# Kernel optimization log

Hardware: AMD Instinct MI355X
Metric: run time of the kernel (lower is better)

Reference implementation:

```python
import jax, jax.numpy as jnp
import numpy as np

DIM = 1024
INTER = 1408
N_EXPERTS = 16
TOPK = 2
N_SHARED = 2
SHARED_INTER = N_SHARED * INTER
ROUTE_SCALE = 1.0


def setup_inputs() -> dict:
    key = jax.random.key(0)
    ks = jax.random.split(key, 16)
    s = 0.02
    return {
        "x": jax.random.normal(ks[0], (2, 2048, DIM), dtype=jnp.float32),
        "gate_w": jax.random.normal(ks[1], (DIM, N_EXPERTS), dtype=jnp.float32) * s,
        "gate_b": jnp.zeros((N_EXPERTS,), dtype=jnp.float32),
        "w1": jax.random.normal(ks[2], (N_EXPERTS, DIM, INTER), dtype=jnp.float32) * s,
        "b1": jnp.zeros((N_EXPERTS, INTER), dtype=jnp.float32),
        "w3": jax.random.normal(ks[3], (N_EXPERTS, DIM, INTER), dtype=jnp.float32) * s,
        "b3": jnp.zeros((N_EXPERTS, INTER), dtype=jnp.float32),
        "w2": jax.random.normal(ks[4], (N_EXPERTS, INTER, DIM), dtype=jnp.float32) * s,
        "b2": jnp.zeros((N_EXPERTS, DIM), dtype=jnp.float32),
        "sw1": jax.random.normal(ks[5], (DIM, SHARED_INTER), dtype=jnp.float32) * s,
        "sb1": jax.random.normal(ks[6], (SHARED_INTER,), dtype=jnp.float32) * s,
        "sw3": jax.random.normal(ks[7], (DIM, SHARED_INTER), dtype=jnp.float32) * s,
        "sb3": jax.random.normal(ks[8], (SHARED_INTER,), dtype=jnp.float32) * s,
        "sw2": jax.random.normal(ks[9], (SHARED_INTER, DIM), dtype=jnp.float32) * s,
        "sb2": jax.random.normal(ks[10], (DIM,), dtype=jnp.float32) * s,
    }


def reference(x, gate_w, gate_b, w1, b1, w3, b3, w2, b2, sw1, sb1, sw3, sb3, sw2, sb2):
    shape = x.shape
    xf = x.reshape(-1, DIM)  # [T, D]

    # Gate: softmax scores in fp32, top-k routing
    logits = xf @ gate_w + gate_b  # [T, E]
    scores = jax.nn.softmax(logits.astype(jnp.float32), axis=-1)
    top_vals, top_idx = jax.lax.top_k(scores, TOPK)  # [T, K]
    weights = (top_vals * ROUTE_SCALE).astype(x.dtype)

    # Combine weights per expert: [T, E]; zero for unselected experts
    cw = (jax.nn.one_hot(top_idx, N_EXPERTS, dtype=x.dtype) * weights[..., None]).sum(axis=1)

    # Routed experts (dense-per-expert SwiGLU, masked by combine weights)
    h = jnp.einsum('td,edh->teh', xf, w1) + b1  # [T, E, I]
    g = jnp.einsum('td,edh->teh', xf, w3) + b3
    a = jax.nn.silu(h) * g
    y = jnp.einsum('teh,ehd,te->td', a, w2, cw) + cw @ b2  # [T, D]

    # Shared expert SwiGLU
    z = (jax.nn.silu(xf @ sw1 + sb1) * (xf @ sw3 + sb3)) @ sw2 + sb2

    return (y + z).reshape(shape)
```

## Files before the change

### kernel.cpp

```cpp
#include <hip/hip_runtime.h>
#include <cstdint>
#include <cstddef>

#define T_TOKENS 4096
#define DIM      1024
#define INTER    1408
#define NEXP     16
#define SINTER   2816

typedef uint32_t u32;
typedef uint16_t u16;

using s8v = __attribute__((ext_vector_type(8))) short;
using f4v = __attribute__((ext_vector_type(4))) float;

__device__ __forceinline__ u16 f2bf(float f) {
  u32 u = __float_as_uint(f);
  return (u16)((u + 0x7fffu + ((u >> 16) & 1u)) >> 16);
}
__device__ __forceinline__ u32 pack2(float a, float b) {
  return (u32)f2bf(a) | ((u32)f2bf(b) << 16);
}

__device__ __forceinline__ void load_lds16(const u16* g, u16* l) {
  __builtin_amdgcn_global_load_lds((const __attribute__((address_space(1))) void*)g,
                                   (__attribute__((address_space(3))) void*)l,
                                   16, 0, 0);
}

__global__ __launch_bounds__(256)
void cvt_x(const float* __restrict__ in, u16* __restrict__ out) {
  const int i = (blockIdx.x * 256 + threadIdx.x) * 8;
  float4 a = *(const float4*)(in + i);
  float4 b = *(const float4*)(in + i + 4);
  uint4 o;
  o.x = pack2(a.x, a.y); o.y = pack2(a.z, a.w);
  o.z = pack2(b.x, b.y); o.w = pack2(b.z, b.w);
  *(uint4*)(out + i) = o;
}

__global__ __launch_bounds__(256)
void transpose_cvt(const float* __restrict__ in, u16* __restrict__ out,
                   int K, int N) {
  const size_t eoff = (size_t)blockIdx.z * K * N;
  const int n0 = blockIdx.x * 64, k0 = blockIdx.y * 64;
  __shared__ u16 t[64][72];

  const int tid = threadIdx.x;
  {
    const int r = tid >> 4, c4 = (tid & 15) * 4;
    const float* src = in + eoff + (size_t)k0 * N + n0;
#pragma unroll
    for (int i = 0; i < 4; i++) {
      int row = r + i * 16;
      float4 v = *(const float4*)(src + (size_t)row * N + c4);
      t[c4 + 0][row] = f2bf(v.x);
      t[c4 + 1][row] = f2bf(v.y);
      t[c4 + 2][row] = f2bf(v.z);
      t[c4 + 3][row] = f2bf(v.w);
    }
  }
  __syncthreads();
  {
    const int r = tid >> 3, cc = (tid & 7) * 8;
    u16* dst = out + eoff + (size_t)n0 * K + k0;
#pragma unroll
    for (int i = 0; i < 2; i++) {
      int row = r + i * 32;
      uint4 v = *(const uint4*)&t[row][cc];
      *(uint4*)(dst + (size_t)row * K + cc) = v;
    }
  }
}

__global__ __launch_bounds__(256)
void gate_logits(const float* __restrict__ x, const float* __restrict__ gw,
                 const float* __restrict__ gb,
                 int* __restrict__ g_e, float* __restrict__ g_w)
{
  const int tok  = blockIdx.x * 4 + (threadIdx.x >> 6);
  const int lane = threadIdx.x & 63;
  const int e = lane & 15, s = lane >> 4;
  const float* xr = x + (size_t)tok * DIM;

  float acc = 0.f;
#pragma unroll 8
  for (int i = 0; i < DIM / 4; i++) {
    const int k = i * 4 + s;
    acc = fmaf(xr[k], gw[i * 64 + lane], acc);
  }
  acc += __shfl_xor(acc, 16, 64);
  acc += __shfl_xor(acc, 32, 64);
  const float logit = acc + gb[e];

  float mx = logit;
#pragma unroll
  for (int o = 1; o < 16; o <<= 1) mx = fmaxf(mx, __shfl_xor(mx, o, 64));
  float p = __expf(logit - mx);
  float sum = p;
#pragma unroll
  for (int o = 1; o < 16; o <<= 1) sum += __shfl_xor(sum, o, 64);
  p /= sum;

  float m0 = p; int i0 = e;
#pragma unroll
  for (int o = 1; o < 16; o <<= 1) {
    float om = __shfl_xor(m0, o, 64); int oi = __shfl_xor(i0, o, 64);
    if (om > m0 || (om == m0 && oi < i0)) { m0 = om; i0 = oi; }
  }
  float p1 = (e == i0) ? -1.f : p;
  float m1 = p1; int i1 = e;
#pragma unroll
  for (int o = 1; o < 16; o <<= 1) {
    float om = __shfl_xor(m1, o, 64); int oi = __shfl_xor(i1, o, 64);
    if (om > m1 || (om == m1 && oi < i1)) { m1 = om; i1 = oi; }
  }
  if (lane == 0) {
    g_e[tok * 2 + 0] = i0;  g_e[tok * 2 + 1] = i1;
    g_w[tok * 2 + 0] = m0;  g_w[tok * 2 + 1] = m1;
  }
}

__global__ __launch_bounds__(256)
void route_build(const int* __restrict__ g_e, const float* __restrict__ g_w,
                 int* __restrict__ offsets,
                 int* __restrict__ tok_slot, float* __restrict__ w_slot)
{
  __shared__ int hist[256][NEXP + 1];
  __shared__ int base[NEXP + 1];
  const int tid = threadIdx.x;
  const int TPT = T_TOKENS / 256;
  const int t0 = tid * TPT;

#pragma unroll
  for (int e = 0; e < NEXP; e++) hist[tid][e] = 0;
  for (int t = t0; t < t0 + TPT; t++) {
    hist[tid][g_e[t * 2 + 0]]++;
    hist[tid][g_e[t * 2 + 1]]++;
  }
  __syncthreads();
  if (tid < NEXP) {
    int run = 0;
    for (int i = 0; i < 256; i++) { int v = hist[i][tid]; hist[i][tid] = run; run += v; }
    base[tid] = run;
  }
  __syncthreads();
  if (tid == 0) {
    int run = 0;
#pragma unroll
    for (int e = 0; e < NEXP; e++) { int c = base[e]; base[e] = run; offsets[e] = run; run += c; }
    base[NEXP] = run; offsets[NEXP] = run;
  }
  __syncthreads();
  for (int t = t0; t < t0 + TPT; t++) {
#pragma unroll
    for (int k = 0; k < 2; k++) {
      const int e = g_e[t * 2 + k];
      const int slot = base[e] + hist[tid][e]++;
      tok_slot[slot] = t;
      w_slot[slot] = g_w[t * 2 + k];
    }
  }
}

template<bool GATHER>
__global__ __launch_bounds__(256, 2)
void ffn_up2(const u16* __restrict__ xbf,
             const u16* __restrict__ w1t, const float* __restrict__ b1p,
             const u16* __restrict__ w3t, const float* __restrict__ b3p,
             int N,
             const int* __restrict__ offsets, const int* __restrict__ tok_slot,
             u16* __restrict__ act)
{
  int e = 0, rowbase = 0, count = T_TOKENS;
  if constexpr (GATHER) {
    e = blockIdx.z; rowbase = offsets[e]; count = offsets[e + 1] - rowbase;
  }
  const int m0 = blockIdx.y * 128;
  if (m0 >= count) return;
  const int n0 = blockIdx.x * 128;

  const u16* W1 = w1t + (size_t)e * N * DIM;
  const u16* W3 = w3t + (size_t)e * N * DIM;
  const float* B1 = b1p + (size_t)e * N;
  const float* B3 = b3p + (size_t)e * N;

  __shared__ u16 sA[128 * 32];
  __shared__ u16 sB1[128 * 32];
  __shared__ u16 sB3[128 * 32];

  const int tid = threadIdx.x;
  const int lane = tid & 63;
  const int w = tid >> 6;

  const int kc8 = (lane & 3) * 8;
  const u16* aptr[2]; const u16* b1ptr[2]; const u16* b3ptr[2];
  u16 *ldsA[2], *ldsB1[2], *ldsB3[2];
#pragma unroll
  for (int i = 0; i < 2; i++) {
    const int row = i * 64 + w * 16 + (lane >> 2);
    const int ldoff = i * 2048 + w * 512 + lane * 8;
    ldsA[i] = sA + ldoff; ldsB1[i] = sB1 + ldoff; ldsB3[i] = sB3 + ldoff;
    int arow = m0 + row; if (arow > count - 1) arow = count - 1;
    const int tok = GATHER ? tok_slot[rowbase + arow] : arow;
    aptr[i]  = xbf + (size_t)tok * DIM + kc8;
    const int brow = n0 + row;
    b1ptr[i] = W1 + (size_t)brow * DIM + kc8;
    b3ptr[i] = W3 + (size_t)brow * DIM + kc8;
  }

  const int ln = lane & 15, q = lane >> 4;
  const int wm = (w & 1) * 64, wn = (w >> 1) * 64;
  const u16* pa  = sA  + (wm + ln) * 32 + q * 8;
  const u16* pb1 = sB1 + (wn + ln) * 32 + q * 8;
  const u16* pb3 = sB3 + (wn + ln) * 32 + q * 8;

  f4v acc1[4][4] = {};
  f4v acc3[4][4] = {};

  for (int k0 = 0; k0 < DIM; k0 += 32) {
    __syncthreads();
#pragma unroll
    for (int i = 0; i < 2; i++) {
      load_lds16(aptr[i]  + k0, ldsA[i]);
      load_lds16(b1ptr[i] + k0, ldsB1[i]);
      load_lds16(b3ptr[i] + k0, ldsB3[i]);
    }
    __syncthreads();

    s8v af[4];
#pragma unroll
    for (int i = 0; i < 4; i++) af[i] = *(const s8v*)(pa + i * 512);
#pragma unroll
    for (int j = 0; j < 4; j++) {
      s8v bf1 = *(const s8v*)(pb1 + j * 512);
#pragma unroll
      for (int i = 0; i < 4; i++)
        acc1[i][j] = __builtin_amdgcn_mfma_f32_16x16x32_bf16(af[i], bf1, acc1[i][j], 0, 0, 0);
      s8v bf3 = *(const s8v*)(pb3 + j * 512);
#pragma unroll
      for (int i = 0; i < 4; i++)
        acc3[i][j] = __builtin_amdgcn_mfma_f32_16x16x32_bf16(af[i], bf3, acc3[i][j], 0, 0, 0);
    }
  }

  float bb1[4], bb3[4];
#pragma unroll
  for (int j = 0; j < 4; j++) {
    const int col = n0 + wn + j * 16 + ln;
    bb1[j] = B1[col]; bb3[j] = B3[col];
  }
#pragma unroll
  for (int i = 0; i < 4; i++) {
#pragma unroll
    for (int r = 0; r < 4; r++) {
      const int row = m0 + wm + i * 16 + q * 4 + r;
      if (row >= count) continue;
      u16* ap = act + (size_t)(rowbase + row) * N + n0 + wn;
#pragma unroll
      for (int j = 0; j < 4; j++) {
        float h = acc1[i][j][r] + bb1[j];
        float g = acc3[i][j][r] + bb3[j];
        float sv = 1.f / (1.f + __expf(-h));
        ap[j * 16 + ln] = f2bf(h * sv * g);
      }
    }
  }
}

template<bool SCATTER>
__global__ __launch_bounds__(256, 2)
void ffn_down2(const u16* __restrict__ act, int KA,
               const u16* __restrict__ w2t, const float* __restrict__ b2p,
               const int* __restrict__ offsets, const int* __restrict__ tok_slot,
               const float* __restrict__ w_slot, float* __restrict__ out)
{
  int e = 0, rowbase = 0, count = T_TOKENS;
  if constexpr (SCATTER) {
    e = blockIdx.z; rowbase = offsets[e]; count = offsets[e + 1] - rowbase;
  }
  const int m0 = blockIdx.y * 128;
  if (m0 >= count) return;
  const int n0 = blockIdx.x * 128;

  const u16* W2 = w2t + (size_t)e * DIM * KA;
  const float* B2 = b2p + (size_t)e * DIM;

  __shared__ u16 sA[128 * 32];
  __shared__ u16 sB[128 * 32];

  const int tid = threadIdx.x;
  const int lane = tid & 63;
  const int w = tid >> 6;

  const int kc8 = (lane & 3) * 8;
  const u16* aptr[2]; const u16* bptr[2];
  u16 *ldsA[2], *ldsB[2];
#pragma unroll
  for (int i = 0; i < 2; i++) {
    const int row = i * 64 + w * 16 + (lane >> 2);
    const int ldoff = i * 2048 + w * 512 + lane * 8;
    ldsA[i] = sA + ldoff; ldsB[i] = sB + ldoff;
    int arow = m0 + row; if (arow > count - 1) arow = count - 1;
    aptr[i] = act + (size_t)(rowbase + arow) * KA + kc8;
    bptr[i] = W2 + (size_t)(n0 + row) * KA + kc8;
  }

  const int ln = lane & 15, q = lane >> 4;
  const int wm = (w & 1) * 64, wn = (w >> 1) * 64;
  const u16* pa = sA + (wm + ln) * 32 + q * 8;
  const u16* pb = sB + (wn + ln) * 32 + q * 8;

  f4v acc[4][4] = {};

  for (int k0 = 0; k0 < KA; k0 += 32) {
    __syncthreads();
#pragma unroll
    for (int i = 0; i < 2; i++) {
      load_lds16(aptr[i] + k0, ldsA[i]);
      load_lds16(bptr[i] + k0, ldsB[i]);
    }
    __syncthreads();

    s8v af[4];
#pragma unroll
    for (int i = 0; i < 4; i++) af[i] = *(const s8v*)(pa + i * 512);
#pragma unroll
    for (int j = 0; j < 4; j++) {
      s8v bf = *(const s8v*)(pb + j * 512);
#pragma unroll
      for (int i = 0; i < 4; i++)
        acc[i][j] = __builtin_amdgcn_mfma_f32_16x16x32_bf16(af[i], bf, acc[i][j], 0, 0, 0);
    }
  }

  float bb[4];
#pragma unroll
  for (int j = 0; j < 4; j++) bb[j] = B2[n0 + wn + j * 16 + ln];

#pragma unroll
  for (int i = 0; i < 4; i++) {
#pragma unroll
    for (int r = 0; r < 4; r++) {
      const int row = m0 + wm + i * 16 + q * 4 + r;
      if (row >= count) continue;
      if constexpr (SCATTER) {
        const int slot = rowbase + row;
        const int tok = tok_slot[slot];
        const float wgt = w_slot[slot];
        float* orow = out + (size_t)tok * DIM + n0 + wn;
#pragma unroll
        for (int j = 0; j < 4; j++)
          atomicAdd(&orow[j * 16 + ln], wgt * (acc[i][j][r] + bb[j]));
      } else {
        float* orow = out + (size_t)row * DIM + n0 + wn;
#pragma unroll
        for (int j = 0; j < 4; j++)
          orow[j * 16 + ln] = acc[i][j][r] + bb[j];
      }
    }
  }
}

extern "C" void kernel_launch(void* const* d_in, const int* in_sizes, int n_in,
                              void* d_out, int out_size, void* d_ws, size_t ws_size,
                              hipStream_t stream)
{
  const float* x   = (const float*)d_in[0];
  const float* gw  = (const float*)d_in[1];
  const float* gb  = (const float*)d_in[2];
  const float* w1  = (const float*)d_in[3];
  const float* b1  = (const float*)d_in[4];
  const float* w3  = (const float*)d_in[5];
  const float* b3  = (const float*)d_in[6];
  const float* w2  = (const float*)d_in[7];
  const float* b2  = (const float*)d_in[8];
  const float* sw1 = (const float*)d_in[9];
  const float* sb1 = (const float*)d_in[10];
  const float* sw3 = (const float*)d_in[11];
  const float* sb3 = (const float*)d_in[12];
  const float* sw2 = (const float*)d_in[13];
  const float* sb2 = (const float*)d_in[14];
  float* out = (float*)d_out;

  char* ws = (char*)d_ws;
  size_t off = 0;
  auto alloc = [&](size_t bytes) -> char* {
    off = (off + 255) & ~(size_t)255;
    char* p = ws + off;
    off += bytes;
    return p;
  };
  int*   offsets  = (int*)  alloc((NEXP + 1) * 4);
  int*   g_e      = (int*)  alloc((size_t)T_TOKENS * 2 * 4);
  float* g_w      = (float*)alloc((size_t)T_TOKENS * 2 * 4);
  int*   tok_slot = (int*)  alloc((size_t)T_TOKENS * 2 * 4);
  float* w_slot   = (float*)alloc((size_t)T_TOKENS * 2 * 4);
  u16*   xbf      = (u16*)  alloc((size_t)T_TOKENS * DIM * 2);
  u16*   w1t      = (u16*)  alloc((size_t)NEXP * INTER * DIM * 2);
  u16*   w3t      = (u16*)  alloc((size_t)NEXP * INTER * DIM * 2);
  u16*   w2t      = (u16*)  alloc((size_t)NEXP * DIM * INTER * 2);
  u16*   sw1t     = (u16*)  alloc((size_t)SINTER * DIM * 2);
  u16*   sw3t     = (u16*)  alloc((size_t)SINTER * DIM * 2);
  u16*   sw2t     = (u16*)  alloc((size_t)DIM * SINTER * 2);
  u16*   A_act    = (u16*)  alloc((size_t)T_TOKENS * 2 * INTER * 2);
  u16*   S_act    = (u16*)  alloc((size_t)T_TOKENS * SINTER * 2);
  (void)ws_size; (void)in_sizes; (void)n_in; (void)out_size;

  gate_logits<<<T_TOKENS / 4, 256, 0, stream>>>(x, gw, gb, g_e, g_w);
  route_build<<<1, 256, 0, stream>>>(g_e, g_w, offsets, tok_slot, w_slot);

  cvt_x<<<(T_TOKENS * DIM) / (256 * 8), 256, 0, stream>>>(x, xbf);
  transpose_cvt<<<dim3(INTER / 64, DIM / 64, NEXP), 256, 0, stream>>>(w1, w1t, DIM, INTER);
  transpose_cvt<<<dim3(INTER / 64, DIM / 64, NEXP), 256, 0, stream>>>(w3, w3t, DIM, INTER);
  transpose_cvt<<<dim3(DIM / 64, INTER / 64, NEXP), 256, 0, stream>>>(w2, w2t, INTER, DIM);
  transpose_cvt<<<dim3(SINTER / 64, DIM / 64, 1), 256, 0, stream>>>(sw1, sw1t, DIM, SINTER);
  transpose_cvt<<<dim3(SINTER / 64, DIM / 64, 1), 256, 0, stream>>>(sw3, sw3t, DIM, SINTER);
  transpose_cvt<<<dim3(DIM / 64, SINTER / 64, 1), 256, 0, stream>>>(sw2, sw2t, SINTER, DIM);

  ffn_up2<false><<<dim3(SINTER / 128, T_TOKENS / 128, 1), 256, 0, stream>>>(
      xbf, sw1t, sb1, sw3t, sb3, SINTER, nullptr, nullptr, S_act);
  ffn_down2<false><<<dim3(DIM / 128, T_TOKENS / 128, 1), 256, 0, stream>>>(
      S_act, SINTER, sw2t, sb2, nullptr, nullptr, nullptr, out);

  ffn_up2<true><<<dim3(INTER / 128, T_TOKENS / 128, NEXP), 256, 0, stream>>>(
      xbf, w1t, b1, w3t, b3, INTER, offsets, tok_slot, A_act);
  ffn_down2<true><<<dim3(DIM / 128, T_TOKENS / 128, NEXP), 256, 0, stream>>>(
      A_act, INTER, w2t, b2, offsets, tok_slot, w_slot, out);
}
```

Measured before the change: 694.3 us.

## Double-buffer LDS in FFN GEMMs, remap blocks per XCD, replace atomics with combine

```diff
diff --git a/kernel.cpp b/kernel.cpp
--- a/kernel.cpp
+++ b/kernel.cpp
@@ -122,9 +122,9 @@
 }
 
 __global__ __launch_bounds__(256)
-void route_build(const int* __restrict__ g_e, const float* __restrict__ g_w,
+void route_build(const int* __restrict__ g_e,
                  int* __restrict__ offsets,
-                 int* __restrict__ tok_slot, float* __restrict__ w_slot)
+                 int* __restrict__ tok_slot, int* __restrict__ slot_of)
 {
   __shared__ int hist[256][NEXP + 1];
   __shared__ int base[NEXP + 1];
@@ -158,7 +158,7 @@
       const int e = g_e[t * 2 + k];
       const int slot = base[e] + hist[tid][e]++;
       tok_slot[slot] = t;
-      w_slot[slot] = g_w[t * 2 + k];
+      slot_of[t * 2 + k] = slot;
     }
   }
 }
@@ -172,22 +172,37 @@
              const int* __restrict__ offsets, const int* __restrict__ tok_slot,
              u16* __restrict__ act)
 {
-  int e = 0, rowbase = 0, count = T_TOKENS;
-  if constexpr (GATHER) {
-    e = blockIdx.z; rowbase = offsets[e]; count = offsets[e + 1] - rowbase;
-  }
-  const int m0 = blockIdx.y * 128;
+  int e = 0, n0, mt;
+  {
+    const int lin = blockIdx.x;
+    const int per = gridDim.x >> 3;
+    const int xcd = lin & 7, pos = lin >> 3;
+    if constexpr (GATHER) {
+      const int half = per >> 1;
+      const int sub = (pos >= half) ? 1 : 0;
+      e = xcd * 2 + sub;
+      const int idx = pos - sub * half;
+      n0 = (idx >> 5) * 128;
+      mt = idx & 31;
+    } else {
+      const int g = xcd * per + pos;
+      n0 = (g >> 5) * 128;
+      mt = g & 31;
+    }
+  }
+  int rowbase = 0, count = T_TOKENS;
+  if constexpr (GATHER) { rowbase = offsets[e]; count = offsets[e + 1] - rowbase; }
+  const int m0 = mt * 128;
   if (m0 >= count) return;
-  const int n0 = blockIdx.x * 128;
 
   const u16* W1 = w1t + (size_t)e * N * DIM;
   const u16* W3 = w3t + (size_t)e * N * DIM;
   const float* B1 = b1p + (size_t)e * N;
   const float* B3 = b3p + (size_t)e * N;
 
-  __shared__ u16 sA[128 * 32];
-  __shared__ u16 sB1[128 * 32];
-  __shared__ u16 sB3[128 * 32];
+  __shared__ u16 sA[2][128 * 32];
+  __shared__ u16 sB1[2][128 * 32];
+  __shared__ u16 sB3[2][128 * 32];
 
   const int tid = threadIdx.x;
   const int lane = tid & 63;
@@ -195,12 +210,11 @@
 
   const int kc8 = (lane & 3) * 8;
   const u16* aptr[2]; const u16* b1ptr[2]; const u16* b3ptr[2];
-  u16 *ldsA[2], *ldsB1[2], *ldsB3[2];
+  int ldoff[2];
 #pragma unroll
   for (int i = 0; i < 2; i++) {
     const int row = i * 64 + w * 16 + (lane >> 2);
-    const int ldoff = i * 2048 + w * 512 + lane * 8;
-    ldsA[i] = sA + ldoff; ldsB1[i] = sB1 + ldoff; ldsB3[i] = sB3 + ldoff;
+    ldoff[i] = i * 2048 + w * 512 + lane * 8;
     int arow = m0 + row; if (arow > count - 1) arow = count - 1;
     const int tok = GATHER ? tok_slot[rowbase + arow] : arow;
     aptr[i]  = xbf + (size_t)tok * DIM + kc8;
@@ -211,23 +225,30 @@
 
   const int ln = lane & 15, q = lane >> 4;
   const int wm = (w & 1) * 64, wn = (w >> 1) * 64;
-  const u16* pa  = sA  + (wm + ln) * 32 + q * 8;
-  const u16* pb1 = sB1 + (wn + ln) * 32 + q * 8;
-  const u16* pb3 = sB3 + (wn + ln) * 32 + q * 8;
+  const int paOff = (wm + ln) * 32 + q * 8;
+  const int pbOff = (wn + ln) * 32 + q * 8;
 
   f4v acc1[4][4] = {};
   f4v acc3[4][4] = {};
 
-  for (int k0 = 0; k0 < DIM; k0 += 32) {
-    __syncthreads();
+  auto stage = [&](int buf, int k0) {
 #pragma unroll
     for (int i = 0; i < 2; i++) {
-      load_lds16(aptr[i]  + k0, ldsA[i]);
-      load_lds16(b1ptr[i] + k0, ldsB1[i]);
-      load_lds16(b3ptr[i] + k0, ldsB3[i]);
-    }
-    __syncthreads();
-
+      load_lds16(aptr[i]  + k0, &sA[buf][ldoff[i]]);
+      load_lds16(b1ptr[i] + k0, &sB1[buf][ldoff[i]]);
+      load_lds16(b3ptr[i] + k0, &sB3[buf][ldoff[i]]);
+    }
+  };
+
+  stage(0, 0);
+  __syncthreads();
+  int cur = 0;
+  for (int k0 = 32; k0 <= DIM; k0 += 32) {
+    if (k0 < DIM) stage(cur ^ 1, k0);
+
+    const u16* pa  = sA[cur]  + paOff;
+    const u16* pb1 = sB1[cur] + pbOff;
+    const u16* pb3 = sB3[cur] + pbOff;
     s8v af[4];
 #pragma unroll
     for (int i = 0; i < 4; i++) af[i] = *(const s8v*)(pa + i * 512);
@@ -242,6 +263,8 @@
       for (int i = 0; i < 4; i++)
         acc3[i][j] = __builtin_amdgcn_mfma_f32_16x16x32_bf16(af[i], bf3, acc3[i][j], 0, 0, 0);
     }
+    __syncthreads();
+    cur ^= 1;
   }
 
   float bb1[4], bb3[4];
@@ -268,26 +291,41 @@
   }
 }
 
-template<bool SCATTER>
+template<bool ROUTED>
 __global__ __launch_bounds__(256, 2)
 void ffn_down2(const u16* __restrict__ act, int KA,
                const u16* __restrict__ w2t, const float* __restrict__ b2p,
-               const int* __restrict__ offsets, const int* __restrict__ tok_slot,
-               const float* __restrict__ w_slot, float* __restrict__ out)
-{
-  int e = 0, rowbase = 0, count = T_TOKENS;
-  if constexpr (SCATTER) {
-    e = blockIdx.z; rowbase = offsets[e]; count = offsets[e + 1] - rowbase;
-  }
-  const int m0 = blockIdx.y * 128;
+               const int* __restrict__ offsets,
+               float* __restrict__ outp)
+{
+  int e = 0, n0, mt;
+  {
+    const int lin = blockIdx.x;
+    const int per = gridDim.x >> 3;
+    const int xcd = lin & 7, pos = lin >> 3;
+    if constexpr (ROUTED) {
+      const int half = per >> 1;
+      const int sub = (pos >= half) ? 1 : 0;
+      e = xcd * 2 + sub;
+      const int idx = pos - sub * half;
+      n0 = (idx >> 5) * 128;
+      mt = idx & 31;
+    } else {
+      const int g = xcd * per + pos;
+      n0 = (g >> 5) * 128;
+      mt = g & 31;
+    }
+  }
+  int rowbase = 0, count = T_TOKENS;
+  if constexpr (ROUTED) { rowbase = offsets[e]; count = offsets[e + 1] - rowbase; }
+  const int m0 = mt * 128;
   if (m0 >= count) return;
-  const int n0 = blockIdx.x * 128;
 
   const u16* W2 = w2t + (size_t)e * DIM * KA;
   const float* B2 = b2p + (size_t)e * DIM;
 
-  __shared__ u16 sA[128 * 32];
-  __shared__ u16 sB[128 * 32];
+  __shared__ u16 sA[2][128 * 32];
+  __shared__ u16 sB[2][128 * 32];
 
   const int tid = threadIdx.x;
   const int lane = tid & 63;
@@ -295,12 +333,11 @@
 
   const int kc8 = (lane & 3) * 8;
   const u16* aptr[2]; const u16* bptr[2];
-  u16 *ldsA[2], *ldsB[2];
+  int ldoff[2];
 #pragma unroll
   for (int i = 0; i < 2; i++) {
     const int row = i * 64 + w * 16 + (lane >> 2);
-    const int ldoff = i * 2048 + w * 512 + lane * 8;
-    ldsA[i] = sA + ldoff; ldsB[i] = sB + ldoff;
+    ldoff[i] = i * 2048 + w * 512 + lane * 8;
     int arow = m0 + row; if (arow > count - 1) arow = count - 1;
     aptr[i] = act + (size_t)(rowbase + arow) * KA + kc8;
     bptr[i] = W2 + (size_t)(n0 + row) * KA + kc8;
@@ -308,20 +345,27 @@
 
   const int ln = lane & 15, q = lane >> 4;
   const int wm = (w & 1) * 64, wn = (w >> 1) * 64;
-  const u16* pa = sA + (wm + ln) * 32 + q * 8;
-  const u16* pb = sB + (wn + ln) * 32 + q * 8;
+  const int paOff = (wm + ln) * 32 + q * 8;
+  const int pbOff = (wn + ln) * 32 + q * 8;
 
   f4v acc[4][4] = {};
 
-  for (int k0 = 0; k0 < KA; k0 += 32) {
-    __syncthreads();
+  auto stage = [&](int buf, int k0) {
 #pragma unroll
     for (int i = 0; i < 2; i++) {
-      load_lds16(aptr[i] + k0, ldsA[i]);
-      load_lds16(bptr[i] + k0, ldsB[i]);
-    }
-    __syncthreads();
-
+      load_lds16(aptr[i] + k0, &sA[buf][ldoff[i]]);
+      load_lds16(bptr[i] + k0, &sB[buf][ldoff[i]]);
+    }
+  };
+
+  stage(0, 0);
+  __syncthreads();
+  int cur = 0;
+  for (int k0 = 32; k0 <= KA; k0 += 32) {
+    if (k0 < KA) stage(cur ^ 1, k0);
+
+    const u16* pa = sA[cur] + paOff;
+    const u16* pb = sB[cur] + pbOff;
     s8v af[4];
 #pragma unroll
     for (int i = 0; i < 4; i++) af[i] = *(const s8v*)(pa + i * 512);
@@ -332,6 +376,8 @@
       for (int i = 0; i < 4; i++)
         acc[i][j] = __builtin_amdgcn_mfma_f32_16x16x32_bf16(af[i], bf, acc[i][j], 0, 0, 0);
     }
+    __syncthreads();
+    cur ^= 1;
   }
 
   float bb[4];
@@ -344,22 +390,31 @@
     for (int r = 0; r < 4; r++) {
       const int row = m0 + wm + i * 16 + q * 4 + r;
       if (row >= count) continue;
-      if constexpr (SCATTER) {
-        const int slot = rowbase + row;
-        const int tok = tok_slot[slot];
-        const float wgt = w_slot[slot];
-        float* orow = out + (size_t)tok * DIM + n0 + wn;
-#pragma unroll
-        for (int j = 0; j < 4; j++)
-          atomicAdd(&orow[j * 16 + ln], wgt * (acc[i][j][r] + bb[j]));
-      } else {
-        float* orow = out + (size_t)row * DIM + n0 + wn;
-#pragma unroll
-        for (int j = 0; j < 4; j++)
-          orow[j * 16 + ln] = acc[i][j][r] + bb[j];
-      }
-    }
-  }
+      float* orow = outp + (size_t)(rowbase + row) * DIM + n0 + wn;
+#pragma unroll
+      for (int j = 0; j < 4; j++)
+        orow[j * 16 + ln] = acc[i][j][r] + bb[j];
+    }
+  }
+}
+
+__global__ __launch_bounds__(256)
+void combine(const float* __restrict__ R, const int* __restrict__ slot_of,
+             const float* __restrict__ g_w, float* __restrict__ out)
+{
+  const int t = blockIdx.x;
+  const int c = threadIdx.x * 4;
+  const int s0 = slot_of[t * 2 + 0], s1 = slot_of[t * 2 + 1];
+  const float w0 = g_w[t * 2 + 0],  w1 = g_w[t * 2 + 1];
+  float4 a = *(const float4*)(R + (size_t)s0 * DIM + c);
+  float4 b = *(const float4*)(R + (size_t)s1 * DIM + c);
+  float* op = out + (size_t)t * DIM + c;
+  float4 o = *(const float4*)op;
+  o.x += w0 * a.x + w1 * b.x;
+  o.y += w0 * a.y + w1 * b.y;
+  o.z += w0 * a.z + w1 * b.z;
+  o.w += w0 * a.w + w1 * b.w;
+  *(float4*)op = o;
 }
 
 extern "C" void kernel_launch(void* const* d_in, const int* in_sizes, int n_in,
@@ -395,7 +450,7 @@
   int*   g_e      = (int*)  alloc((size_t)T_TOKENS * 2 * 4);
   float* g_w      = (float*)alloc((size_t)T_TOKENS * 2 * 4);
   int*   tok_slot = (int*)  alloc((size_t)T_TOKENS * 2 * 4);
-  float* w_slot   = (float*)alloc((size_t)T_TOKENS * 2 * 4);
+  int*   slot_of  = (int*)  alloc((size_t)T_TOKENS * 2 * 4);
   u16*   xbf      = (u16*)  alloc((size_t)T_TOKENS * DIM * 2);
   u16*   w1t      = (u16*)  alloc((size_t)NEXP * INTER * DIM * 2);
   u16*   w3t      = (u16*)  alloc((size_t)NEXP * INTER * DIM * 2);
@@ -405,10 +460,11 @@
   u16*   sw2t     = (u16*)  alloc((size_t)DIM * SINTER * 2);
   u16*   A_act    = (u16*)  alloc((size_t)T_TOKENS * 2 * INTER * 2);
   u16*   S_act    = (u16*)  alloc((size_t)T_TOKENS * SINTER * 2);
+  float* Rbuf     = (float*)w1t;
   (void)ws_size; (void)in_sizes; (void)n_in; (void)out_size;
 
   gate_logits<<<T_TOKENS / 4, 256, 0, stream>>>(x, gw, gb, g_e, g_w);
-  route_build<<<1, 256, 0, stream>>>(g_e, g_w, offsets, tok_slot, w_slot);
+  route_build<<<1, 256, 0, stream>>>(g_e, offsets, tok_slot, slot_of);
 
   cvt_x<<<(T_TOKENS * DIM) / (256 * 8), 256, 0, stream>>>(x, xbf);
   transpose_cvt<<<dim3(INTER / 64, DIM / 64, NEXP), 256, 0, stream>>>(w1, w1t, DIM, INTER);
@@ -418,13 +474,14 @@
   transpose_cvt<<<dim3(SINTER / 64, DIM / 64, 1), 256, 0, stream>>>(sw3, sw3t, DIM, SINTER);
   transpose_cvt<<<dim3(DIM / 64, SINTER / 64, 1), 256, 0, stream>>>(sw2, sw2t, SINTER, DIM);
 
-  ffn_up2<false><<<dim3(SINTER / 128, T_TOKENS / 128, 1), 256, 0, stream>>>(
+  ffn_up2<false><<<(SINTER / 128) * 32, 256, 0, stream>>>(
       xbf, sw1t, sb1, sw3t, sb3, SINTER, nullptr, nullptr, S_act);
-  ffn_down2<false><<<dim3(DIM / 128, T_TOKENS / 128, 1), 256, 0, stream>>>(
-      S_act, SINTER, sw2t, sb2, nullptr, nullptr, nullptr, out);
-
-  ffn_up2<true><<<dim3(INTER / 128, T_TOKENS / 128, NEXP), 256, 0, stream>>>(
+  ffn_down2<false><<<(DIM / 128) * 32, 256, 0, stream>>>(
+      S_act, SINTER, sw2t, sb2, nullptr, out);
+
+  ffn_up2<true><<<(INTER / 128) * 32 * NEXP, 256, 0, stream>>>(
       xbf, w1t, b1, w3t, b3, INTER, offsets, tok_slot, A_act);
-  ffn_down2<true><<<dim3(DIM / 128, T_TOKENS / 128, NEXP), 256, 0, stream>>>(
-      A_act, INTER, w2t, b2, offsets, tok_slot, w_slot, out);
-}
+  ffn_down2<true><<<(DIM / 128) * 32 * NEXP, 256, 0, stream>>>(
+      A_act, INTER, w2t, b2, offsets, Rbuf);
+  combine<<<T_TOKENS, 256, 0, stream>>>(Rbuf, slot_of, g_w, out);
+}
```

Result: no change. 699.2 us (+0.7%).
